# Performance work log

Hardware: AMD Instinct MI355X
Metric: run time of the kernel (lower is better)

Reference implementation:

```python
import jax, jax.numpy as jnp
import numpy as np

N_GRAPHS = 2048
BN_EPS = 1e-5


def _lin_init(k, fan_in, fan_out):
    kw, kb = jax.random.split(k)
    s = 1.0 / np.sqrt(fan_in)
    w = jax.random.uniform(kw, (fan_in, fan_out), minval=-s, maxval=s, dtype=jnp.float32)
    b = jax.random.uniform(kb, (fan_out,), minval=-s, maxval=s, dtype=jnp.float32)
    return w, b


def setup_inputs() -> dict:
    key = jax.random.key(0)
    ks = jax.random.split(key, 16)
    N, E, F, H, C = 100000, 600000, 7, 128, 2
    inp = {}
    inp["x"] = jax.random.normal(ks[0], (N, F), dtype=jnp.float32)
    inp["edge_index"] = jax.random.randint(ks[1], (2, E), 0, N)
    inp["edge_attr"] = jax.random.normal(ks[2], (E,), dtype=jnp.float32)  # ignored by GINConv
    inp["batch"] = jnp.sort(jax.random.randint(ks[3], (N,), 0, N_GRAPHS))
    # GINConv inner MLPs: [in, H, H]
    inp["g1_w1"], inp["g1_b1"] = _lin_init(ks[4], F, H)
    inp["g1_w2"], inp["g1_b2"] = _lin_init(ks[5], H, H)
    inp["g2_w1"], inp["g2_b1"] = _lin_init(ks[6], H, H)
    inp["g2_w2"], inp["g2_b2"] = _lin_init(ks[7], H, H)
    inp["g3_w1"], inp["g3_b1"] = _lin_init(ks[8], H, H)
    inp["g3_w2"], inp["g3_b2"] = _lin_init(ks[9], H, H)
    # JumpingKnowledge('cat') projection: 3H -> H
    inp["jk_w"], inp["jk_b"] = _lin_init(ks[10], 3 * H, H)
    # classifier MLP [H, H, C] with batch_norm on hidden layer
    inp["c1_w"], inp["c1_b"] = _lin_init(ks[11], H, H)
    inp["bn_g"] = jnp.ones((H,), jnp.float32)
    inp["bn_b"] = jnp.zeros((H,), jnp.float32)
    inp["c2_w"], inp["c2_b"] = _lin_init(ks[12], H, C)
    return inp


def reference(x, edge_index, edge_attr, batch,
              g1_w1, g1_b1, g1_w2, g1_b2,
              g2_w1, g2_b1, g2_w2, g2_b2,
              g3_w1, g3_b1, g3_w2, g3_b2,
              jk_w, jk_b, c1_w, c1_b, bn_g, bn_b, c2_w, c2_b):
    src, dst = edge_index[0], edge_index[1]
    N = x.shape[0]

    def gin_conv(h, w1, b1, w2, b2):
        # sum aggregation of neighbor messages; eps=0 -> (1+eps)*x + aggr = x + aggr
        agg = jax.ops.segment_sum(h[src], dst, num_segments=N)
        z = h + agg
        return jax.nn.relu(z @ w1 + b1) @ w2 + b2  # inner MLP, plain last layer

    # BasicGNN applies act (ReLU) after each conv; dropout=eval (identity)
    h1 = jax.nn.relu(gin_conv(x, g1_w1, g1_b1, g1_w2, g1_b2))
    h2 = jax.nn.relu(gin_conv(h1, g2_w1, g2_b1, g2_w2, g2_b2))
    h3 = jax.nn.relu(gin_conv(h2, g3_w1, g3_b1, g3_w2, g3_b2))

    h = jnp.concatenate([h1, h2, h3], axis=-1) @ jk_w + jk_b  # jk='cat' + final lin
    g = jax.ops.segment_sum(h, batch, num_segments=N_GRAPHS)  # global_add_pool -> [G, H]

    z = g @ c1_w + c1_b
    mu = z.mean(axis=0)
    var = z.var(axis=0)
    z = (z - mu) * jax.lax.rsqrt(var + BN_EPS) * bn_g + bn_b  # batch_norm (batch stats)
    z = jax.nn.relu(z)
    return z @ c2_w + c2_b  # [G, num_classes]
```

## Files before the change

### kernel.cpp

```cpp
#include <hip/hip_runtime.h>

#define NGRAPH 2048

typedef __attribute__((ext_vector_type(4))) float f32x4;
typedef __attribute__((ext_vector_type(8))) _Float16 h16x8;
typedef __attribute__((ext_vector_type(2))) _Float16 h16x2;

__global__ __launch_bounds__(256) void scan_onepass(
    const int* __restrict__ deg, int* __restrict__ rowstart, int* __restrict__ cursor,
    unsigned* __restrict__ scanst, int N, int E, int nchunk)
{
  __shared__ int tmp[256];
  __shared__ int sh_chunk;
  __shared__ int sh_exc;
  int tid = threadIdx.x;
  if (tid == 0) sh_chunk = (int)atomicAdd(&scanst[nchunk], 1u);
  __syncthreads();
  int cb = sh_chunk;
  int i = cb * 256 + tid;
  int v = (i < N) ? deg[i] : 0;
  tmp[tid] = v;
  __syncthreads();
#pragma unroll
  for (int off = 1; off < 256; off <<= 1) {
    int t = (tid >= off) ? tmp[tid - off] : 0;
    __syncthreads();
    tmp[tid] += t;
    __syncthreads();
  }
  int aggregate = tmp[255];

  if (tid == 0) {
    const unsigned VMASK = (1u << 30) - 1u;
    if (cb == 0) {
      atomicExch(&scanst[0], (2u << 30) | (unsigned)aggregate);
      sh_exc = 0;
    } else {
      atomicExch(&scanst[cb], (1u << 30) | (unsigned)aggregate);
      int excv = 0;
      int j = cb - 1;
      while (j >= 0) {
        unsigned s;
        do { s = atomicAdd(&scanst[j], 0u); } while ((s >> 30) == 0u);
        excv += (int)(s & VMASK);
        if ((s >> 30) == 2u) break;
        --j;
      }
      sh_exc = excv;
      atomicExch(&scanst[cb], (2u << 30) | (unsigned)(excv + aggregate));
    }
  }
  __syncthreads();
  int exc = sh_exc;
  if (i < N) {
    int rs = exc + tmp[tid] - v;
    rowstart[i] = rs;
    cursor[i] = rs;
  }
  if (cb == nchunk - 1 && tid == 0) rowstart[N] = E;
}

__global__ __launch_bounds__(256) void fill_eidx(
    const int* __restrict__ src, const int* __restrict__ dst,
    int* __restrict__ cursor, int* __restrict__ eidx, int E)
{
  int e = blockIdx.x * 256 + threadIdx.x;
  if (e >= E) return;
  int d = dst[e];
  int pos = atomicAdd(&cursor[d], 1);
  eidx[pos] = src[e];
}

struct WPs {
  const float* w[5];
  _Float16* hi[5];
  _Float16* lo[5];
};
__global__ __launch_bounds__(256) void prep_hist(
    WPs p, const float* __restrict__ x, _Float16* __restrict__ x8h, int N,
    const int* __restrict__ dst, int* __restrict__ deg, int E,
    const int* __restrict__ batch, int* __restrict__ gstart,
    float* __restrict__ bnstat)
{
  int g = blockIdx.x * 256 + threadIdx.x;
  if (g < E) {
    atomicAdd(&deg[dst[g]], 1);
    return;
  }
  int q = g - E;
  if (q < 5 * 16384) {
    int m = q >> 14;
    int j = q & 16383;
    int c = j >> 3, e = j & 7;
    int t = c >> 8, kc = (c >> 6) & 3, lane = c & 63;
    int n = t * 16 + (lane & 15);
    int k = kc * 32 + (lane >> 4) * 8 + e;
    float w = p.w[m][k * 128 + n];
    _Float16 h = (_Float16)w;
    p.hi[m][j] = h;
    p.lo[m][j] = (_Float16)(w - (float)h);
    return;
  }
  q -= 5 * 16384;
  if (q < N * 8) {
    int v = q >> 3, j = q & 7;
    x8h[q] = (_Float16)((j < 7) ? x[(long)v * 7 + j] : 0.f);
    return;
  }
  q -= N * 8;
  if (q < 256) { bnstat[q] = 0.f; return; }
  q -= 256;
  if (q < N) {
    int b = batch[q];
    int bp = (q > 0) ? batch[q - 1] : -1;
    for (int gg = bp + 1; gg <= b; ++gg) gstart[gg] = q;
    if (q == N - 1)
      for (int gg = b + 1; gg <= NGRAPH; ++gg) gstart[gg] = N;
  }
}

__device__ inline void mfma_pass(
    const _Float16* __restrict__ zbuf,
    const _Float16* __restrict__ Whi, const _Float16* __restrict__ Wlo,
    int rw, int m16, int quad, int lane, f32x4 acc[8])
{
  int r = rw + m16;
  const _Float16* zrow = &zbuf[r * 128];
#pragma unroll
  for (int kc = 0; kc < 4; ++kc) {
    int cidx = kc * 4 + quad;
    h16x8 ah = *(const h16x8*)&zrow[((cidx + r) & 15) * 8];
#pragma unroll
    for (int t = 0; t < 8; ++t) {
      long cb = ((t * 4 + kc) * 64 + lane) * 8;
      h16x8 bh = *(const h16x8*)&Whi[cb];
      h16x8 bl = *(const h16x8*)&Wlo[cb];
      acc[t] = __builtin_amdgcn_mfma_f32_16x16x32_f16(ah, bh, acc[t], 0, 0, 0);
      acc[t] = __builtin_amdgcn_mfma_f32_16x16x32_f16(ah, bl, acc[t], 0, 0, 0);
    }
  }
}

__global__ __launch_bounds__(256, 8) void fused_gin(
    const _Float16* __restrict__ H, const int* __restrict__ rowstart,
    const int* __restrict__ eidx,
    const _Float16* __restrict__ W1hi, const _Float16* __restrict__ W1lo,
    const float* __restrict__ B1,
    const _Float16* __restrict__ W2hi, const _Float16* __restrict__ W2lo,
    const float* __restrict__ B2,
    _Float16* __restrict__ Out, int M)
{
  __shared__ _Float16 zbuf[64 * 128];
  int tid = threadIdx.x;
  int rbase = blockIdx.x * 64;

  {
    int sub = tid & 15;
    int ng = tid >> 4;
    const _Float16* Hc = H + sub * 8;
#pragma unroll
    for (int it = 0; it < 4; ++it) {
      int r = it * 16 + ng;
      int v = rbase + r;
      int vc = (v < M) ? v : (M - 1);
      h16x8 sv = *(const h16x8*)&Hc[(long)vc * 128];
      float a0[8], a1[8];
#pragma unroll
      for (int j = 0; j < 8; ++j) { a0[j] = (float)sv[j]; a1[j] = 0.f; }
      int e0 = rowstart[vc], e1 = rowstart[vc + 1];
      int e = e0;
      for (; e + 4 <= e1; e += 4) {
        int s0 = eidx[e], s1 = eidx[e + 1], s2 = eidx[e + 2], s3 = eidx[e + 3];
        h16x8 h0 = *(const h16x8*)&Hc[(long)s0 * 128];
        h16x8 h1 = *(const h16x8*)&Hc[(long)s1 * 128];
        h16x8 h2 = *(const h16x8*)&Hc[(long)s2 * 128];
        h16x8 h3 = *(const h16x8*)&Hc[(long)s3 * 128];
#pragma unroll
        for (int j = 0; j < 8; ++j) {
          a0[j] += (float)h0[j] + (float)h2[j];
          a1[j] += (float)h1[j] + (float)h3[j];
        }
      }
      for (; e + 2 <= e1; e += 2) {
        int s0 = eidx[e], s1 = eidx[e + 1];
        h16x8 h0 = *(const h16x8*)&Hc[(long)s0 * 128];
        h16x8 h1 = *(const h16x8*)&Hc[(long)s1 * 128];
#pragma unroll
        for (int j = 0; j < 8; ++j) {
          a0[j] += (float)h0[j];
          a1[j] += (float)h1[j];
        }
      }
      if (e < e1) {
        int s = eidx[e];
        h16x8 h = *(const h16x8*)&Hc[(long)s * 128];
#pragma unroll
        for (int j = 0; j < 8; ++j) a1[j] += (float)h[j];
      }
      h16x8 zo;
#pragma unroll
      for (int j = 0; j < 8; ++j) zo[j] = (_Float16)(a0[j] + a1[j]);
      *(h16x8*)&zbuf[r * 128 + ((sub + r) & 15) * 8] = zo;
    }
  }
  __syncthreads();

  int lane = tid & 63;
  int wv = tid >> 6;
  int m16 = lane & 15;
  int quad = lane >> 4;
  int rw = wv * 16;

  f32x4 acc[8];
#pragma unroll
  for (int t = 0; t < 8; ++t) acc[t] = (f32x4){0.f, 0.f, 0.f, 0.f};
  mfma_pass(zbuf, W1hi, W1lo, rw, m16, quad, lane, acc);

  float bias[8];
#pragma unroll
  for (int t = 0; t < 8; ++t) bias[t] = B1[t * 16 + m16];

  __syncthreads();
#pragma unroll
  for (int i = 0; i < 4; ++i) {
    int r = rw + quad * 4 + i;
#pragma unroll
    for (int t = 0; t < 8; ++t) {
      int col = t * 16 + m16;
      int cidx = col >> 3;
      zbuf[r * 128 + ((cidx + r) & 15) * 8 + (col & 7)] =
          (_Float16)fmaxf(acc[t][i] + bias[t], 0.f);
    }
  }
  __syncthreads();

#pragma unroll
  for (int t = 0; t < 8; ++t) acc[t] = (f32x4){0.f, 0.f, 0.f, 0.f};
  mfma_pass(zbuf, W2hi, W2lo, rw, m16, quad, lane, acc);

#pragma unroll
  for (int t = 0; t < 8; ++t) bias[t] = B2[t * 16 + m16];

#pragma unroll
  for (int i = 0; i < 4; ++i) {
    int r = rbase + rw + quad * 4 + i;
    if (r < M) {
#pragma unroll
      for (int t = 0; t < 8; ++t) {
        float o = fmaxf(acc[t][i] + bias[t], 0.f);
        Out[(long)r * 128 + t * 16 + m16] = (_Float16)o;
      }
    }
  }
}

__global__ __launch_bounds__(256, 8) void fused_l1(
    const _Float16* __restrict__ x8h, const int* __restrict__ rowstart,
    const int* __restrict__ eidx,
    const float* __restrict__ W1, const float* __restrict__ B1,
    const _Float16* __restrict__ W2hi, const _Float16* __restrict__ W2lo,
    const float* __restrict__ B2, _Float16* __restrict__ Out, int M)
{
  __shared__ _Float16 ybuf[64 * 128];
  __shared__ float z1s[64][8];
  int tid = threadIdx.x;
  int rbase = blockIdx.x * 64;

  {
    int node = tid >> 2, sub = tid & 3;
    int v = rbase + node;
    int vc = (v < M) ? v : (M - 1);
    float a[8];
    if (sub == 0) {
      h16x8 sv = *(const h16x8*)&x8h[(long)vc * 8];
#pragma unroll
      for (int j = 0; j < 8; ++j) a[j] = (float)sv[j];
    } else {
#pragma unroll
      for (int j = 0; j < 8; ++j) a[j] = 0.f;
    }
    int e0 = rowstart[vc], e1 = rowstart[vc + 1];
    int e = e0 + sub;
    for (; e + 4 < e1; e += 8) {
      int s0 = eidx[e], s1 = eidx[e + 4];
      h16x8 h0 = *(const h16x8*)&x8h[(long)s0 * 8];
      h16x8 h1 = *(const h16x8*)&x8h[(long)s1 * 8];
#pragma unroll
      for (int j = 0; j < 8; ++j) a[j] += (float)h0[j] + (float)h1[j];
    }
    if (e < e1) {
      int s = eidx[e];
      h16x8 h = *(const h16x8*)&x8h[(long)s * 8];
#pragma unroll
      for (int j = 0; j < 8; ++j) a[j] += (float)h[j];
    }
#pragma unroll
    for (int j = 0; j < 8; ++j) {
      a[j] += __shfl_xor(a[j], 1, 64);
      a[j] += __shfl_xor(a[j], 2, 64);
    }
    if (sub == 0) {
#pragma unroll
      for (int j = 0; j < 8; ++j) z1s[node][j] = a[j];
    }
  }
  __syncthreads();

  {
    int c = tid & 127;
    int cidx = c >> 3, celt = c & 7;
    int rh0 = (tid >> 7) * 32;
    float w1r[7];
#pragma unroll
    for (int k = 0; k < 7; ++k) w1r[k] = W1[k * 128 + c];
    float b1 = B1[c];
#pragma unroll 4
    for (int rr = 0; rr < 32; ++rr) {
      int r = rh0 + rr;
      const float* zp = z1s[r];
      float a = b1;
#pragma unroll
      for (int k = 0; k < 7; ++k) a += zp[k] * w1r[k];
      ybuf[r * 128 + ((cidx + r) & 15) * 8 + celt] = (_Float16)fmaxf(a, 0.f);
    }
  }
  __syncthreads();

  int lane = tid & 63;
  int wv = tid >> 6;
  int m16 = lane & 15;
  int quad = lane >> 4;
  int rw = wv * 16;

  f32x4 acc[8];
#pragma unroll
  for (int t = 0; t < 8; ++t) acc[t] = (f32x4){0.f, 0.f, 0.f, 0.f};
  mfma_pass(ybuf, W2hi, W2lo, rw, m16, quad, lane, acc);

  float bias[8];
#pragma unroll
  for (int t = 0; t < 8; ++t) bias[t] = B2[t * 16 + m16];

#pragma unroll
  for (int i = 0; i < 4; ++i) {
    int r = rbase + rw + quad * 4 + i;
    if (r < M) {
#pragma unroll
      for (int t = 0; t < 8; ++t) {
        float o = fmaxf(acc[t][i] + bias[t], 0.f);
        Out[(long)r * 128 + t * 16 + m16] = (_Float16)o;
      }
    }
  }
}

__global__ __launch_bounds__(256) void pool_direct(
    const _Float16* __restrict__ H1, const _Float16* __restrict__ H2,
    const _Float16* __restrict__ H3, const int* __restrict__ gstart,
    float* __restrict__ P, float* __restrict__ cnt)
{
  int g = blockIdx.x;
  int s = gstart[g], e = gstart[g + 1];
  int tid = threadIdx.x;
  if (tid == 0) cnt[g] = (float)(e - s);
  if (tid >= 192) return;
  int cp = tid * 2;
  const _Float16* A = (cp < 128) ? H1 : ((cp < 256) ? H2 : H3);
  int c = cp & 127;
  float ax = 0.f, ay = 0.f, bx = 0.f, by = 0.f;
  int i = s;
  for (; i + 2 <= e; i += 2) {
    h16x2 v0 = *(const h16x2*)&A[(long)i * 128 + c];
    h16x2 v1 = *(const h16x2*)&A[(long)(i + 1) * 128 + c];
    ax += (float)v0[0]; ay += (float)v0[1];
    bx += (float)v1[0]; by += (float)v1[1];
  }
  if (i < e) {
    h16x2 v0 = *(const h16x2*)&A[(long)i * 128 + c];
    ax += (float)v0[0]; ay += (float)v0[1];
  }
  float2 o = {ax + bx, ay + by};
  *(float2*)&P[(long)g * 384 + cp] = o;
}

__global__ __launch_bounds__(256) void jk_gemm(
    const float* __restrict__ P, const float* __restrict__ cnt,
    const float* __restrict__ W, const float* __restrict__ B,
    float* __restrict__ G)
{
  __shared__ float pl[768];
  int tid = threadIdx.x, blk = blockIdx.x;
  for (int o = tid; o < 768; o += 256) pl[o] = P[(long)blk * 768 + o];
  __syncthreads();
  int rr = tid >> 7;
  int col = tid & 127;
  int row = blk * 2 + rr;
  float acc = cnt[row] * B[col];
#pragma unroll 8
  for (int k = 0; k < 384; ++k)
    acc += pl[rr * 384 + k] * W[k * 128 + col];
  G[(long)row * 128 + col] = acc;
}

__global__ __launch_bounds__(256) void gemm_bn(
    const float* __restrict__ Z,
    const float* __restrict__ W, const float* __restrict__ B,
    float* __restrict__ Out, float* __restrict__ bnstat, int M)
{
  __shared__ float wlds[128 * 128];
  int tid = threadIdx.x;
  {
    const float4* Ws = (const float4*)W;
    float4* Wd = (float4*)wlds;
#pragma unroll
    for (int i = 0; i < 16; ++i) Wd[i * 256 + tid] = Ws[i * 256 + tid];
  }
  __syncthreads();

  int rg = tid >> 5;
  int c0 = (tid & 31) * 4;
  int rbase = blockIdx.x * 64 + rg * 8;

  float acc[8][4];
#pragma unroll
  for (int i = 0; i < 8; ++i)
#pragma unroll
    for (int j = 0; j < 4; ++j) acc[i][j] = 0.f;

#pragma unroll 2
  for (int kc = 0; kc < 128; kc += 4) {
    float zv[8][4];
#pragma unroll
    for (int i = 0; i < 8; ++i) {
      float4 z = *(const float4*)&Z[(long)(rbase + i) * 128 + kc];
      zv[i][0] = z.x; zv[i][1] = z.y; zv[i][2] = z.z; zv[i][3] = z.w;
    }
#pragma unroll
    for (int kk = 0; kk < 4; ++kk) {
      float4 w = *(const float4*)&wlds[(kc + kk) * 128 + c0];
#pragma unroll
      for (int i = 0; i < 8; ++i) {
        float z = zv[i][kk];
        acc[i][0] += z * w.x; acc[i][1] += z * w.y;
        acc[i][2] += z * w.z; acc[i][3] += z * w.w;
      }
    }
  }

  float4 b = *(const float4*)&B[c0];
  float s[4] = {0.f, 0.f, 0.f, 0.f};
  float s2[4] = {0.f, 0.f, 0.f, 0.f};
#pragma unroll
  for (int i = 0; i < 8; ++i) {
    float4 o;
    o.x = acc[i][0] + b.x; o.y = acc[i][1] + b.y;
    o.z = acc[i][2] + b.z; o.w = acc[i][3] + b.w;
    *(float4*)&Out[(long)(rbase + i) * 128 + c0] = o;
    s[0] += o.x; s[1] += o.y; s[2] += o.z; s[3] += o.w;
    s2[0] += o.x * o.x; s2[1] += o.y * o.y; s2[2] += o.z * o.z; s2[3] += o.w * o.w;
  }
#pragma unroll
  for (int j = 0; j < 4; ++j) {
    atomicAdd(&bnstat[c0 + j], s[j]);
    atomicAdd(&bnstat[128 + c0 + j], s2[j]);
  }
}

__global__ __launch_bounds__(256) void bn_final(
    const float* __restrict__ ZC, const float* __restrict__ bnstat,
    const float* __restrict__ gma, const float* __restrict__ bta,
    const float* __restrict__ W2, const float* __restrict__ B2, float* __restrict__ out)
{
  __shared__ float scl[128], shf[128];
  int tid = threadIdx.x;
  if (tid < 128) {
    float mu = bnstat[tid] * (1.f / NGRAPH);
    float var = bnstat[128 + tid] * (1.f / NGRAPH) - mu * mu;
    float rs = rsqrtf(var + 1e-5f);
    float sc = gma[tid] * rs;
    scl[tid] = sc;
    shf[tid] = bta[tid] - mu * sc;
  }
  __syncthreads();
  int g = blockIdx.x * 256 + tid;
  if (g >= NGRAPH) return;
  float a0 = B2[0], a1 = B2[1];
#pragma unroll 4
  for (int h = 0; h < 128; ++h) {
    float zn = ZC[(long)g * 128 + h] * scl[h] + shf[h];
    zn = fmaxf(zn, 0.f);
    a0 += zn * W2[2 * h];
    a1 += zn * W2[2 * h + 1];
  }
  out[2 * g] = a0;
  out[2 * g + 1] = a1;
}

extern "C" void kernel_launch(void* const* d_in, const int* in_sizes, int n_in,
                              void* d_out, int out_size, void* d_ws, size_t ws_size,
                              hipStream_t stream)
{
  const float* x    = (const float*)d_in[0];
  const int*   ei   = (const int*)d_in[1];
  const int*   batch = (const int*)d_in[3];
  const float* g1w1 = (const float*)d_in[4];  const float* g1b1 = (const float*)d_in[5];
  const float* g1w2 = (const float*)d_in[6];  const float* g1b2 = (const float*)d_in[7];
  const float* g2w1 = (const float*)d_in[8];  const float* g2b1 = (const float*)d_in[9];
  const float* g2w2 = (const float*)d_in[10]; const float* g2b2 = (const float*)d_in[11];
  const float* g3w1 = (const float*)d_in[12]; const float* g3b1 = (const float*)d_in[13];
  const float* g3w2 = (const float*)d_in[14]; const float* g3b2 = (const float*)d_in[15];
  const float* jkw  = (const float*)d_in[16]; const float* jkb  = (const float*)d_in[17];
  const float* c1w  = (const float*)d_in[18]; const float* c1b  = (const float*)d_in[19];
  const float* bng  = (const float*)d_in[20]; const float* bnb  = (const float*)d_in[21];
  const float* c2w  = (const float*)d_in[22]; const float* c2b  = (const float*)d_in[23];

  const int N = in_sizes[3];
  const int E = in_sizes[1] / 2;
  const int* src = ei;
  const int* dst = ei + E;

  char* w = (char*)d_ws;
  auto alloc = [&](size_t bytes) {
    char* p = w;
    w += (bytes + 255) & ~(size_t)255;
    return p;
  };
  _Float16* hA = (_Float16*)alloc((size_t)N * 128 * 2);
  _Float16* hB = (_Float16*)alloc((size_t)N * 128 * 2);
  _Float16* hC = (_Float16*)alloc((size_t)N * 128 * 2);
  _Float16* x8h = (_Float16*)alloc((size_t)N * 8 * 2);
  float* P       = (float*)alloc((size_t)NGRAPH * 384 * 4);
  float* cnt     = (float*)alloc((size_t)NGRAPH * 4);
  float* bnstat  = (float*)alloc(256 * 4);
  float* gbuf = (float*)alloc((size_t)NGRAPH * 128 * 4);
  float* zc   = (float*)alloc((size_t)NGRAPH * 128 * 4);
  int* deg      = (int*)alloc((size_t)N * 4);
  unsigned* scanst = (unsigned*)alloc((size_t)1024 * 4);
  int* cursor   = (int*)alloc((size_t)N * 4);
  int* rowstart = (int*)alloc((size_t)(N + 1) * 4);
  int* eidx     = (int*)alloc((size_t)E * 4);
  int* gstart   = (int*)alloc((size_t)(NGRAPH + 1) * 4);
  _Float16* wtbuf = (_Float16*)alloc((size_t)5 * 2 * 16384 * 2);

  _Float16* WThi[5];
  _Float16* WTlo[5];
  for (int m = 0; m < 5; ++m) {
    WThi[m] = wtbuf + (size_t)m * 2 * 16384;
    WTlo[m] = WThi[m] + 16384;
  }

  const int nchunk = (N + 255) / 256;
  const int eb = (E + 255) / 256;

  hipMemsetAsync(deg, 0, (size_t)((char*)(scanst + 1024) - (char*)deg), stream);

  {
    WPs p;
    p.w[0] = g1w2; p.w[1] = g2w1; p.w[2] = g2w2; p.w[3] = g3w1; p.w[4] = g3w2;
    for (int m = 0; m < 5; ++m) { p.hi[m] = WThi[m]; p.lo[m] = WTlo[m]; }
    int total = E + 5 * 16384 + N * 8 + 256 + N;
    prep_hist<<<(total + 255) / 256, 256, 0, stream>>>(p, x, x8h, N, dst, deg, E,
                                                       batch, gstart, bnstat);
  }

  scan_onepass<<<nchunk, 256, 0, stream>>>(deg, rowstart, cursor, scanst, N, E, nchunk);
  fill_eidx<<<eb, 256, 0, stream>>>(src, dst, cursor, eidx, E);

  const int fBlocks = (N + 63) / 64;

  fused_l1<<<fBlocks, 256, 0, stream>>>(x8h, rowstart, eidx, g1w1, g1b1,
      WThi[0], WTlo[0], g1b2, hC, N);
  fused_gin<<<fBlocks, 256, 0, stream>>>(hC, rowstart, eidx,
      WThi[1], WTlo[1], g2b1, WThi[2], WTlo[2], g2b2, hB, N);
  fused_gin<<<fBlocks, 256, 0, stream>>>(hB, rowstart, eidx,
      WThi[3], WTlo[3], g3b1, WThi[4], WTlo[4], g3b2, hA, N);

  pool_direct<<<NGRAPH, 256, 0, stream>>>(hC, hB, hA, gstart, P, cnt);

  jk_gemm<<<NGRAPH / 2, 256, 0, stream>>>(P, cnt, jkw, jkb, gbuf);
  gemm_bn<<<NGRAPH / 64, 256, 0, stream>>>(gbuf, c1w, c1b, zc, bnstat, NGRAPH);
  bn_final<<<(NGRAPH + 255) / 256, 256, 0, stream>>>(zc, bnstat, bng, bnb, c2w, c2b, (float*)d_out);
}
```

Measured before the change: 401.9 us.

## Stage edge indices in LDS, widen masked gather, coalesce output stores

In fused_gin, each 64-row block now loads its rowstart slice and its edge-index slice into shared memory once, when the slice fits in 1024 entries. The neighbor gather then runs an 8-wide masked loop reading indices from LDS, which puts more independent H-row loads in flight per iteration; blocks whose slice does not fit keep a global-index path. Both fused kernels now stage their final output in LDS and write it as 16-byte vector stores per row instead of scattered 2-byte stores. Two block barriers are dropped because each wave only touches its own rows, and the occupancy hint falls from 8 to 5. The masked loop issues redundant loads for rows with low degree, and the extra shared memory plus the lower occupancy hint may cost occupancy.

```diff
diff --git a/kernel.cpp b/kernel.cpp
--- a/kernel.cpp
+++ b/kernel.cpp
@@ -1,6 +1,7 @@
 #include <hip/hip_runtime.h>
 
 #define NGRAPH 2048
+#define EIDX_CAP 1024
 
 typedef __attribute__((ext_vector_type(4))) float f32x4;
 typedef __attribute__((ext_vector_type(8))) _Float16 h16x8;
@@ -141,7 +142,7 @@
   }
 }
 
-__global__ __launch_bounds__(256, 8) void fused_gin(
+__global__ __launch_bounds__(256, 5) void fused_gin(
     const _Float16* __restrict__ H, const int* __restrict__ rowstart,
     const int* __restrict__ eidx,
     const _Float16* __restrict__ W1hi, const _Float16* __restrict__ W1lo,
@@ -151,56 +152,105 @@
     _Float16* __restrict__ Out, int M)
 {
   __shared__ _Float16 zbuf[64 * 128];
+  __shared__ int sh_rs[65];
+  __shared__ int sh_ei[EIDX_CAP];
   int tid = threadIdx.x;
   int rbase = blockIdx.x * 64;
+
+  if (tid < 65) {
+    int v = rbase + tid;
+    sh_rs[tid] = rowstart[(v < M) ? v : M];
+  }
+  __syncthreads();
+  int e_begin = sh_rs[0];
+  int cnt = sh_rs[64] - e_begin;
+  if (cnt <= EIDX_CAP) {
+    for (int i = tid; i < cnt; i += 256) sh_ei[i] = eidx[e_begin + i];
+  }
+  __syncthreads();
 
   {
     int sub = tid & 15;
     int ng = tid >> 4;
     const _Float16* Hc = H + sub * 8;
-#pragma unroll
-    for (int it = 0; it < 4; ++it) {
-      int r = it * 16 + ng;
-      int v = rbase + r;
-      int vc = (v < M) ? v : (M - 1);
-      h16x8 sv = *(const h16x8*)&Hc[(long)vc * 128];
-      float a0[8], a1[8];
-#pragma unroll
-      for (int j = 0; j < 8; ++j) { a0[j] = (float)sv[j]; a1[j] = 0.f; }
-      int e0 = rowstart[vc], e1 = rowstart[vc + 1];
-      int e = e0;
-      for (; e + 4 <= e1; e += 4) {
-        int s0 = eidx[e], s1 = eidx[e + 1], s2 = eidx[e + 2], s3 = eidx[e + 3];
-        h16x8 h0 = *(const h16x8*)&Hc[(long)s0 * 128];
-        h16x8 h1 = *(const h16x8*)&Hc[(long)s1 * 128];
-        h16x8 h2 = *(const h16x8*)&Hc[(long)s2 * 128];
-        h16x8 h3 = *(const h16x8*)&Hc[(long)s3 * 128];
-#pragma unroll
-        for (int j = 0; j < 8; ++j) {
-          a0[j] += (float)h0[j] + (float)h2[j];
-          a1[j] += (float)h1[j] + (float)h3[j];
+    if (cnt <= EIDX_CAP) {
+#pragma unroll 1
+      for (int it = 0; it < 4; ++it) {
+        int r = it * 16 + ng;
+        int v = rbase + r;
+        int vc = (v < M) ? v : (M - 1);
+        h16x8 sv = *(const h16x8*)&Hc[(long)vc * 128];
+        float a0[8], a1[8];
+#pragma unroll
+        for (int j = 0; j < 8; ++j) { a0[j] = (float)sv[j]; a1[j] = 0.f; }
+        int e = sh_rs[r] - e_begin;
+        int e1 = sh_rs[r + 1] - e_begin;
+#pragma unroll 1
+        for (; e < e1; e += 8) {
+          int last = e1 - 1;
+          int s0 = sh_ei[e];
+          int s1 = sh_ei[(e + 1 < e1) ? e + 1 : last];
+          int s2 = sh_ei[(e + 2 < e1) ? e + 2 : last];
+          int s3 = sh_ei[(e + 3 < e1) ? e + 3 : last];
+          int s4 = sh_ei[(e + 4 < e1) ? e + 4 : last];
+          int s5 = sh_ei[(e + 5 < e1) ? e + 5 : last];
+          int s6 = sh_ei[(e + 6 < e1) ? e + 6 : last];
+          int s7 = sh_ei[(e + 7 < e1) ? e + 7 : last];
+          float m1 = (e + 1 < e1) ? 1.f : 0.f;
+          float m2 = (e + 2 < e1) ? 1.f : 0.f;
+          float m3 = (e + 3 < e1) ? 1.f : 0.f;
+          float m4 = (e + 4 < e1) ? 1.f : 0.f;
+          float m5 = (e + 5 < e1) ? 1.f : 0.f;
+          float m6 = (e + 6 < e1) ? 1.f : 0.f;
+          float m7 = (e + 7 < e1) ? 1.f : 0.f;
+          h16x8 h0 = *(const h16x8*)&Hc[(long)s0 * 128];
+          h16x8 h1 = *(const h16x8*)&Hc[(long)s1 * 128];
+          h16x8 h2 = *(const h16x8*)&Hc[(long)s2 * 128];
+          h16x8 h3 = *(const h16x8*)&Hc[(long)s3 * 128];
+          h16x8 h4 = *(const h16x8*)&Hc[(long)s4 * 128];
+          h16x8 h5 = *(const h16x8*)&Hc[(long)s5 * 128];
+          h16x8 h6 = *(const h16x8*)&Hc[(long)s6 * 128];
+          h16x8 h7 = *(const h16x8*)&Hc[(long)s7 * 128];
+#pragma unroll
+          for (int j = 0; j < 8; ++j) {
+            a0[j] += (float)h0[j] + m2 * (float)h2[j] + m4 * (float)h4[j] + m6 * (float)h6[j];
+            a1[j] += m1 * (float)h1[j] + m3 * (float)h3[j] + m5 * (float)h5[j] + m7 * (float)h7[j];
+          }
         }
+        h16x8 zo;
+#pragma unroll
+        for (int j = 0; j < 8; ++j) zo[j] = (_Float16)(a0[j] + a1[j]);
+        *(h16x8*)&zbuf[r * 128 + ((sub + r) & 15) * 8] = zo;
       }
-      for (; e + 2 <= e1; e += 2) {
-        int s0 = eidx[e], s1 = eidx[e + 1];
-        h16x8 h0 = *(const h16x8*)&Hc[(long)s0 * 128];
-        h16x8 h1 = *(const h16x8*)&Hc[(long)s1 * 128];
-#pragma unroll
-        for (int j = 0; j < 8; ++j) {
-          a0[j] += (float)h0[j];
-          a1[j] += (float)h1[j];
+    } else {
+#pragma unroll 1
+      for (int it = 0; it < 4; ++it) {
+        int r = it * 16 + ng;
+        int v = rbase + r;
+        int vc = (v < M) ? v : (M - 1);
+        h16x8 sv = *(const h16x8*)&Hc[(long)vc * 128];
+        float a0[8], a1[8];
+#pragma unroll
+        for (int j = 0; j < 8; ++j) { a0[j] = (float)sv[j]; a1[j] = 0.f; }
+        int e = sh_rs[r], e1 = sh_rs[r + 1];
+        for (; e + 2 <= e1; e += 2) {
+          int s0 = eidx[e], s1 = eidx[e + 1];
+          h16x8 h0 = *(const h16x8*)&Hc[(long)s0 * 128];
+          h16x8 h1 = *(const h16x8*)&Hc[(long)s1 * 128];
+#pragma unroll
+          for (int j = 0; j < 8; ++j) { a0[j] += (float)h0[j]; a1[j] += (float)h1[j]; }
         }
+        if (e < e1) {
+          int s = eidx[e];
+          h16x8 h = *(const h16x8*)&Hc[(long)s * 128];
+#pragma unroll
+          for (int j = 0; j < 8; ++j) a1[j] += (float)h[j];
+        }
+        h16x8 zo;
+#pragma unroll
+        for (int j = 0; j < 8; ++j) zo[j] = (_Float16)(a0[j] + a1[j]);
+        *(h16x8*)&zbuf[r * 128 + ((sub + r) & 15) * 8] = zo;
       }
-      if (e < e1) {
-        int s = eidx[e];
-        h16x8 h = *(const h16x8*)&Hc[(long)s * 128];
-#pragma unroll
-        for (int j = 0; j < 8; ++j) a1[j] += (float)h[j];
-      }
-      h16x8 zo;
-#pragma unroll
-      for (int j = 0; j < 8; ++j) zo[j] = (_Float16)(a0[j] + a1[j]);
-      *(h16x8*)&zbuf[r * 128 + ((sub + r) & 15) * 8] = zo;
     }
   }
   __syncthreads();
@@ -220,7 +270,6 @@
 #pragma unroll
   for (int t = 0; t < 8; ++t) bias[t] = B1[t * 16 + m16];
 
-  __syncthreads();
 #pragma unroll
   for (int i = 0; i < 4; ++i) {
     int r = rw + quad * 4 + i;
@@ -232,7 +281,6 @@
           (_Float16)fmaxf(acc[t][i] + bias[t], 0.f);
     }
   }
-  __syncthreads();
 
 #pragma unroll
   for (int t = 0; t < 8; ++t) acc[t] = (f32x4){0.f, 0.f, 0.f, 0.f};
@@ -243,12 +291,24 @@
 
 #pragma unroll
   for (int i = 0; i < 4; ++i) {
-    int r = rbase + rw + quad * 4 + i;
+    int r = rw + quad * 4 + i;
+#pragma unroll
+    for (int t = 0; t < 8; ++t) {
+      int col = t * 16 + m16;
+      int cidx = col >> 3;
+      zbuf[r * 128 + ((cidx + r) & 15) * 8 + (col & 7)] =
+          (_Float16)fmaxf(acc[t][i] + bias[t], 0.f);
+    }
+  }
+  {
+    int rr2 = tid >> 2, c4 = tid & 3;
+    int r = rbase + rr2;
     if (r < M) {
 #pragma unroll
-      for (int t = 0; t < 8; ++t) {
-        float o = fmaxf(acc[t][i] + bias[t], 0.f);
-        Out[(long)r * 128 + t * 16 + m16] = (_Float16)o;
+      for (int it = 0; it < 4; ++it) {
+        int cidx = it * 4 + c4;
+        h16x8 vv = *(const h16x8*)&zbuf[rr2 * 128 + ((cidx + rr2) & 15) * 8];
+        *(h16x8*)&Out[(long)r * 128 + cidx * 8] = vv;
       }
     }
   }
@@ -343,12 +403,24 @@
 
 #pragma unroll
   for (int i = 0; i < 4; ++i) {
-    int r = rbase + rw + quad * 4 + i;
+    int r = rw + quad * 4 + i;
+#pragma unroll
+    for (int t = 0; t < 8; ++t) {
+      int col = t * 16 + m16;
+      int cidx = col >> 3;
+      ybuf[r * 128 + ((cidx + r) & 15) * 8 + (col & 7)] =
+          (_Float16)fmaxf(acc[t][i] + bias[t], 0.f);
+    }
+  }
+  {
+    int rr2 = tid >> 2, c4 = tid & 3;
+    int r = rbase + rr2;
     if (r < M) {
 #pragma unroll
-      for (int t = 0; t < 8; ++t) {
-        float o = fmaxf(acc[t][i] + bias[t], 0.f);
-        Out[(long)r * 128 + t * 16 + m16] = (_Float16)o;
+      for (int it = 0; it < 4; ++it) {
+        int cidx = it * 4 + c4;
+        h16x8 vv = *(const h16x8*)&ybuf[rr2 * 128 + ((cidx + rr2) & 15) * 8];
+        *(h16x8*)&Out[(long)r * 128 + cidx * 8] = vv;
       }
     }
   }
```

After: 413.3 us. +2.8%, slower.

## Split GIN layers into slice-wise gather and MLP kernels over a column-sliced layout

Applied to the files above, without the earlier changes.

Node features are now stored as 8 column slices of 16 halves each, so each slice is a contiguous N×16 array. A new gather_slice kernel aggregates neighbours one slice at a time, so the random gather touches a working set small enough to stay cache-resident. mlp_tile then reads the aggregated slices and runs the two MFMA GEMMs, and writes its output back in the sliced layout through LDS. The pooling kernel is adapted to the new layout. The cost is an extra write and read of the full aggregate buffer per layer and one more kernel launch per layer.

```diff
diff --git a/kernel.cpp b/kernel.cpp
--- a/kernel.cpp
+++ b/kernel.cpp
@@ -141,72 +141,87 @@
   }
 }
 
-__global__ __launch_bounds__(256, 8) void fused_gin(
-    const _Float16* __restrict__ H, const int* __restrict__ rowstart,
-    const int* __restrict__ eidx,
+__global__ __launch_bounds__(256) void gather_slice(
+    const _Float16* __restrict__ Hs, const int* __restrict__ rowstart,
+    const int* __restrict__ eidx, _Float16* __restrict__ zS, int N, int C)
+{
+  int bid = blockIdx.x;
+  int s = bid & 7;
+  int chunk = bid >> 3;
+  int start = chunk * C;
+  int end = start + C;
+  if (end > N) end = N;
+  int tid = threadIdx.x;
+  const _Float16* __restrict__ Hsl = Hs + (size_t)s * N * 16;
+  _Float16* __restrict__ zsl = zS + (size_t)s * N * 16;
+  int half8 = (tid & 1) * 8;
+
+  for (int v = start + (tid >> 1); v < end; v += 128) {
+    h16x8 sv = *(const h16x8*)&Hsl[(size_t)v * 16 + half8];
+    float a0[8], a1[8];
+#pragma unroll
+    for (int j = 0; j < 8; ++j) { a0[j] = (float)sv[j]; a1[j] = 0.f; }
+    int e0 = __builtin_nontemporal_load(&rowstart[v]);
+    int e1 = __builtin_nontemporal_load(&rowstart[v + 1]);
+#pragma unroll 1
+    for (int e = e0; e < e1; e += 4) {
+      int last = e1 - 1;
+      int p1 = (e + 1 < e1) ? e + 1 : last;
+      int p2 = (e + 2 < e1) ? e + 2 : last;
+      int p3 = (e + 3 < e1) ? e + 3 : last;
+      int i0 = __builtin_nontemporal_load(&eidx[e]);
+      int i1 = __builtin_nontemporal_load(&eidx[p1]);
+      int i2 = __builtin_nontemporal_load(&eidx[p2]);
+      int i3 = __builtin_nontemporal_load(&eidx[p3]);
+      float m1 = (e + 1 < e1) ? 1.f : 0.f;
+      float m2 = (e + 2 < e1) ? 1.f : 0.f;
+      float m3 = (e + 3 < e1) ? 1.f : 0.f;
+      h16x8 h0 = *(const h16x8*)&Hsl[(size_t)i0 * 16 + half8];
+      h16x8 h1 = *(const h16x8*)&Hsl[(size_t)i1 * 16 + half8];
+      h16x8 h2 = *(const h16x8*)&Hsl[(size_t)i2 * 16 + half8];
+      h16x8 h3 = *(const h16x8*)&Hsl[(size_t)i3 * 16 + half8];
+#pragma unroll
+      for (int j = 0; j < 8; ++j) {
+        a0[j] += (float)h0[j] + m2 * (float)h2[j];
+        a1[j] += m1 * (float)h1[j] + m3 * (float)h3[j];
+      }
+    }
+    h16x8 zo;
+#pragma unroll
+    for (int j = 0; j < 8; ++j) zo[j] = (_Float16)(a0[j] + a1[j]);
+    __builtin_nontemporal_store(zo, (h16x8*)&zsl[(size_t)v * 16 + half8]);
+  }
+}
+
+__global__ __launch_bounds__(256, 8) void mlp_tile(
+    const _Float16* __restrict__ zS,
     const _Float16* __restrict__ W1hi, const _Float16* __restrict__ W1lo,
     const float* __restrict__ B1,
     const _Float16* __restrict__ W2hi, const _Float16* __restrict__ W2lo,
     const float* __restrict__ B2,
-    _Float16* __restrict__ Out, int M)
+    _Float16* __restrict__ OutS, int M)
 {
   __shared__ _Float16 zbuf[64 * 128];
   int tid = threadIdx.x;
   int rbase = blockIdx.x * 64;
-
-  {
-    int sub = tid & 15;
-    int ng = tid >> 4;
-    const _Float16* Hc = H + sub * 8;
-#pragma unroll
-    for (int it = 0; it < 4; ++it) {
-      int r = it * 16 + ng;
-      int v = rbase + r;
-      int vc = (v < M) ? v : (M - 1);
-      h16x8 sv = *(const h16x8*)&Hc[(long)vc * 128];
-      float a0[8], a1[8];
-#pragma unroll
-      for (int j = 0; j < 8; ++j) { a0[j] = (float)sv[j]; a1[j] = 0.f; }
-      int e0 = rowstart[vc], e1 = rowstart[vc + 1];
-      int e = e0;
-      for (; e + 4 <= e1; e += 4) {
-        int s0 = eidx[e], s1 = eidx[e + 1], s2 = eidx[e + 2], s3 = eidx[e + 3];
-        h16x8 h0 = *(const h16x8*)&Hc[(long)s0 * 128];
-        h16x8 h1 = *(const h16x8*)&Hc[(long)s1 * 128];
-        h16x8 h2 = *(const h16x8*)&Hc[(long)s2 * 128];
-        h16x8 h3 = *(const h16x8*)&Hc[(long)s3 * 128];
-#pragma unroll
-        for (int j = 0; j < 8; ++j) {
-          a0[j] += (float)h0[j] + (float)h2[j];
-          a1[j] += (float)h1[j] + (float)h3[j];
-        }
-      }
-      for (; e + 2 <= e1; e += 2) {
-        int s0 = eidx[e], s1 = eidx[e + 1];
-        h16x8 h0 = *(const h16x8*)&Hc[(long)s0 * 128];
-        h16x8 h1 = *(const h16x8*)&Hc[(long)s1 * 128];
-#pragma unroll
-        for (int j = 0; j < 8; ++j) {
-          a0[j] += (float)h0[j];
-          a1[j] += (float)h1[j];
-        }
-      }
-      if (e < e1) {
-        int s = eidx[e];
-        h16x8 h = *(const h16x8*)&Hc[(long)s * 128];
-#pragma unroll
-        for (int j = 0; j < 8; ++j) a1[j] += (float)h[j];
-      }
-      h16x8 zo;
-#pragma unroll
-      for (int j = 0; j < 8; ++j) zo[j] = (_Float16)(a0[j] + a1[j]);
-      *(h16x8*)&zbuf[r * 128 + ((sub + r) & 15) * 8] = zo;
-    }
-  }
-  __syncthreads();
-
   int lane = tid & 63;
   int wv = tid >> 6;
+
+#pragma unroll
+  for (int it = 0; it < 4; ++it) {
+    int s = wv * 2 + (it >> 1);
+    int part = it & 1;
+    int rloc = part * 32 + (lane >> 1);
+    int half = lane & 1;
+    int r = rbase + rloc;
+    int rc = (r < M) ? r : (M - 1);
+    h16x8 vv = __builtin_nontemporal_load(
+        (const h16x8*)&zS[((size_t)s * M + rc) * 16 + half * 8]);
+    int cidx = s * 2 + half;
+    *(h16x8*)&zbuf[rloc * 128 + ((cidx + rloc) & 15) * 8] = vv;
+  }
+  __syncthreads();
+
   int m16 = lane & 15;
   int quad = lane >> 4;
   int rw = wv * 16;
@@ -220,7 +235,6 @@
 #pragma unroll
   for (int t = 0; t < 8; ++t) bias[t] = B1[t * 16 + m16];
 
-  __syncthreads();
 #pragma unroll
   for (int i = 0; i < 4; ++i) {
     int r = rw + quad * 4 + i;
@@ -232,7 +246,6 @@
           (_Float16)fmaxf(acc[t][i] + bias[t], 0.f);
     }
   }
-  __syncthreads();
 
 #pragma unroll
   for (int t = 0; t < 8; ++t) acc[t] = (f32x4){0.f, 0.f, 0.f, 0.f};
@@ -243,12 +256,25 @@
 
 #pragma unroll
   for (int i = 0; i < 4; ++i) {
-    int r = rbase + rw + quad * 4 + i;
+    int r = rw + quad * 4 + i;
+#pragma unroll
+    for (int t = 0; t < 8; ++t) {
+      int col = t * 16 + m16;
+      int cidx = col >> 3;
+      zbuf[r * 128 + ((cidx + r) & 15) * 8 + (col & 7)] =
+          (_Float16)fmaxf(acc[t][i] + bias[t], 0.f);
+    }
+  }
+  {
+    int rr2 = tid >> 2, c4 = tid & 3;
+    int r = rbase + rr2;
     if (r < M) {
 #pragma unroll
-      for (int t = 0; t < 8; ++t) {
-        float o = fmaxf(acc[t][i] + bias[t], 0.f);
-        Out[(long)r * 128 + t * 16 + m16] = (_Float16)o;
+      for (int it = 0; it < 4; ++it) {
+        int cidx = it * 4 + c4;
+        h16x8 vv = *(const h16x8*)&zbuf[rr2 * 128 + ((cidx + rr2) & 15) * 8];
+        __builtin_nontemporal_store(
+            vv, (h16x8*)&OutS[((size_t)(cidx >> 1) * M + r) * 16 + (cidx & 1) * 8]);
       }
     }
   }
@@ -259,7 +285,7 @@
     const int* __restrict__ eidx,
     const float* __restrict__ W1, const float* __restrict__ B1,
     const _Float16* __restrict__ W2hi, const _Float16* __restrict__ W2lo,
-    const float* __restrict__ B2, _Float16* __restrict__ Out, int M)
+    const float* __restrict__ B2, _Float16* __restrict__ OutS, int M)
 {
   __shared__ _Float16 ybuf[64 * 128];
   __shared__ float z1s[64][8];
@@ -343,21 +369,34 @@
 
 #pragma unroll
   for (int i = 0; i < 4; ++i) {
-    int r = rbase + rw + quad * 4 + i;
+    int r = rw + quad * 4 + i;
+#pragma unroll
+    for (int t = 0; t < 8; ++t) {
+      int col = t * 16 + m16;
+      int cidx = col >> 3;
+      ybuf[r * 128 + ((cidx + r) & 15) * 8 + (col & 7)] =
+          (_Float16)fmaxf(acc[t][i] + bias[t], 0.f);
+    }
+  }
+  {
+    int rr2 = tid >> 2, c4 = tid & 3;
+    int r = rbase + rr2;
     if (r < M) {
 #pragma unroll
-      for (int t = 0; t < 8; ++t) {
-        float o = fmaxf(acc[t][i] + bias[t], 0.f);
-        Out[(long)r * 128 + t * 16 + m16] = (_Float16)o;
+      for (int it = 0; it < 4; ++it) {
+        int cidx = it * 4 + c4;
+        h16x8 vv = *(const h16x8*)&ybuf[rr2 * 128 + ((cidx + rr2) & 15) * 8];
+        __builtin_nontemporal_store(
+            vv, (h16x8*)&OutS[((size_t)(cidx >> 1) * M + r) * 16 + (cidx & 1) * 8]);
       }
     }
   }
 }
 
-__global__ __launch_bounds__(256) void pool_direct(
+__global__ __launch_bounds__(256) void pool_slice(
     const _Float16* __restrict__ H1, const _Float16* __restrict__ H2,
     const _Float16* __restrict__ H3, const int* __restrict__ gstart,
-    float* __restrict__ P, float* __restrict__ cnt)
+    float* __restrict__ P, float* __restrict__ cnt, int N)
 {
   int g = blockIdx.x;
   int s = gstart[g], e = gstart[g + 1];
@@ -367,16 +406,17 @@
   int cp = tid * 2;
   const _Float16* A = (cp < 128) ? H1 : ((cp < 256) ? H2 : H3);
   int c = cp & 127;
+  const _Float16* base = A + ((size_t)(c >> 4) * N) * 16 + (c & 15);
   float ax = 0.f, ay = 0.f, bx = 0.f, by = 0.f;
   int i = s;
   for (; i + 2 <= e; i += 2) {
-    h16x2 v0 = *(const h16x2*)&A[(long)i * 128 + c];
-    h16x2 v1 = *(const h16x2*)&A[(long)(i + 1) * 128 + c];
+    h16x2 v0 = *(const h16x2*)&base[(size_t)i * 16];
+    h16x2 v1 = *(const h16x2*)&base[(size_t)(i + 1) * 16];
     ax += (float)v0[0]; ay += (float)v0[1];
     bx += (float)v1[0]; by += (float)v1[1];
   }
   if (i < e) {
-    h16x2 v0 = *(const h16x2*)&A[(long)i * 128 + c];
+    h16x2 v0 = *(const h16x2*)&base[(size_t)i * 16];
     ax += (float)v0[0]; ay += (float)v0[1];
   }
   float2 o = {ax + bx, ay + by};
@@ -528,6 +568,7 @@
   _Float16* hA = (_Float16*)alloc((size_t)N * 128 * 2);
   _Float16* hB = (_Float16*)alloc((size_t)N * 128 * 2);
   _Float16* hC = (_Float16*)alloc((size_t)N * 128 * 2);
+  _Float16* zS = (_Float16*)alloc((size_t)N * 128 * 2);
   _Float16* x8h = (_Float16*)alloc((size_t)N * 8 * 2);
   float* P       = (float*)alloc((size_t)NGRAPH * 384 * 4);
   float* cnt     = (float*)alloc((size_t)NGRAPH * 4);
@@ -567,15 +608,20 @@
   fill_eidx<<<eb, 256, 0, stream>>>(src, dst, cursor, eidx, E);
 
   const int fBlocks = (N + 63) / 64;
+  const int C = (N + 127) / 128;
 
   fused_l1<<<fBlocks, 256, 0, stream>>>(x8h, rowstart, eidx, g1w1, g1b1,
       WThi[0], WTlo[0], g1b2, hC, N);
-  fused_gin<<<fBlocks, 256, 0, stream>>>(hC, rowstart, eidx,
-      WThi[1], WTlo[1], g2b1, WThi[2], WTlo[2], g2b2, hB, N);
-  fused_gin<<<fBlocks, 256, 0, stream>>>(hB, rowstart, eidx,
-      WThi[3], WTlo[3], g3b1, WThi[4], WTlo[4], g3b2, hA, N);
-
-  pool_direct<<<NGRAPH, 256, 0, stream>>>(hC, hB, hA, gstart, P, cnt);
+
+  gather_slice<<<1024, 256, 0, stream>>>(hC, rowstart, eidx, zS, N, C);
+  mlp_tile<<<fBlocks, 256, 0, stream>>>(zS, WThi[1], WTlo[1], g2b1,
+      WThi[2], WTlo[2], g2b2, hB, N);
+
+  gather_slice<<<1024, 256, 0, stream>>>(hB, rowstart, eidx, zS, N, C);
+  mlp_tile<<<fBlocks, 256, 0, stream>>>(zS, WThi[3], WTlo[3], g3b1,
+      WThi[4], WTlo[4], g3b2, hA, N);
+
+  pool_slice<<<NGRAPH, 256, 0, stream>>>(hC, hB, hA, gstart, P, cnt, N);
 
   jk_gemm<<<NGRAPH / 2, 256, 0, stream>>>(P, cnt, jkw, jkb, gbuf);
   gemm_bn<<<NGRAPH / 64, 256, 0, stream>>>(gbuf, c1w, c1b, zc, bnstat, NGRAPH);
```

Result: slower. 533.2 us (+32.7%).
